# Performance work log

Measured on AMD Instinct MI355X. Metric: run time of the kernel, lower is better.

## Reference

```python
import jax, jax.numpy as jnp
import numpy as np

B, S, L = 512, 512, 128


def setup_inputs() -> dict:
    key = jax.random.key(0)
    k1, k2, k3, k4 = jax.random.split(key, 4)
    return {
        "input": jax.random.normal(k1, (B, S, L), dtype=jnp.float32),
        "label": jax.random.randint(k2, (B, S), 0, L),
        "length": jax.random.randint(k3, (B,), 1, S + 1),
        "trans": jax.random.uniform(k4, (L, L), dtype=jnp.float32),
    }


def reference(input, label, length, trans):
    b, s, l = input.shape
    length = jnp.clip(length, 1, s)
    # sequence mask [B, S]
    mask = (jnp.arange(s)[None, :] < length[:, None]).astype(input.dtype)
    x = input * mask[:, :, None]  # masked emissions, as in call()

    # --- gold path score (compute_path_score, via gathers instead of dense one-hot outer products) ---
    point_score = jnp.sum(
        jnp.take_along_axis(x, label[:, :, None], axis=2)[:, :, 0] * mask,
        axis=1, keepdims=True)
    pair_mask = mask[:, :-1] * mask[:, 1:]
    trans_score = jnp.sum(trans[label[:, :-1], label[:, 1:]] * pair_mask,
                          axis=1, keepdims=True)
    label_score = point_score + trans_score  # [B, 1]

    # --- forward algorithm (comput_z recurrence) as lax.scan ---
    def step(alpha, xt):
        # alpha: [B, L] prev forward vars; xt: [B, L] emissions at t
        alpha = jax.nn.logsumexp(alpha[:, :, None] + trans[None, :, :], axis=1) + xt
        return alpha, alpha

    alpha0 = x[:, 0, :]
    xs = jnp.swapaxes(x, 0, 1)[1:]  # [S-1, B, L]
    _, alphas = jax.lax.scan(step, alpha0, xs)
    alphas = jnp.concatenate([alpha0[None], alphas], axis=0)  # [S, B, L]

    # pick forward vars at the last valid position of each sequence
    final_scores = alphas[length - 1, jnp.arange(b)]  # [B, L]
    z = jax.nn.logsumexp(final_scores, axis=1, keepdims=True)  # [B, 1]
    return z - label_score
```

## Files before the change

kernel.cpp:

```cpp
#include <hip/hip_runtime.h>

#define BB 512
#define SS 512
#define LL 128

__global__ void __launch_bounds__(256) crf_label_score_kernel(
    const float* __restrict__ input, const int* __restrict__ label,
    const int* __restrict__ length, const float* __restrict__ trans,
    float* __restrict__ ls)
{
    const int b = blockIdx.x;
    const int tid = threadIdx.x;
    int len = length[b];
    len = len < 1 ? 1 : (len > SS ? SS : len);

    float acc = 0.f;
    for (int t = tid; t < len; t += 256) {
        const int lab = label[b * SS + t];
        acc += input[((size_t)b * SS + t) * LL + lab];
        if (t + 1 < len) {
            const int lab2 = label[b * SS + t + 1];
            acc += trans[lab * LL + lab2];
        }
    }
    #pragma unroll
    for (int off = 32; off > 0; off >>= 1) acc += __shfl_xor(acc, off, 64);
    __shared__ float wpart[4];
    if ((tid & 63) == 0) wpart[tid >> 6] = acc;
    __syncthreads();
    if (tid == 0) ls[b] = wpart[0] + wpart[1] + wpart[2] + wpart[3];
}

__global__ void __launch_bounds__(128) crf_forward_kernel(
    const float* __restrict__ input, const int* __restrict__ length,
    const float* __restrict__ trans, const float* __restrict__ ls,
    float* __restrict__ out)
{
    const int b = blockIdx.x;
    const int j = threadIdx.x;
    int len = length[b];
    len = len < 1 ? 1 : (len > SS ? SS : len);

    __shared__ float e_lds[LL];
    __shared__ float wred[2];
    __shared__ float wsum[2];

    float tcol[LL];
    #pragma unroll
    for (int i = 0; i < LL; ++i)
        tcol[i] = __expf(trans[i * LL + j]);

    const float* __restrict__ xb = input + (size_t)b * SS * LL;
    float alpha = xb[j];

    for (int t = 1; t < len; ++t) {
        const float xt = xb[t * LL + j];

        float m = alpha;
        #pragma unroll
        for (int off = 32; off > 0; off >>= 1) m = fmaxf(m, __shfl_xor(m, off, 64));
        if ((j & 63) == 0) wred[j >> 6] = m;
        __syncthreads();
        const float M = fmaxf(wred[0], wred[1]);

        e_lds[j] = __expf(alpha - M);
        __syncthreads();

        float acc0 = 0.f, acc1 = 0.f, acc2 = 0.f, acc3 = 0.f;
        const float4* __restrict__ e4 = reinterpret_cast<const float4*>(e_lds);
        #pragma unroll
        for (int i = 0; i < LL / 4; ++i) {
            const float4 ev = e4[i];
            acc0 = fmaf(ev.x, tcol[4 * i + 0], acc0);
            acc1 = fmaf(ev.y, tcol[4 * i + 1], acc1);
            acc2 = fmaf(ev.z, tcol[4 * i + 2], acc2);
            acc3 = fmaf(ev.w, tcol[4 * i + 3], acc3);
        }
        alpha = M + __logf((acc0 + acc1) + (acc2 + acc3)) + xt;
    }

    float m = alpha;
    #pragma unroll
    for (int off = 32; off > 0; off >>= 1) m = fmaxf(m, __shfl_xor(m, off, 64));
    if ((j & 63) == 0) wred[j >> 6] = m;
    __syncthreads();
    const float M = fmaxf(wred[0], wred[1]);

    float ex = __expf(alpha - M);
    #pragma unroll
    for (int off = 32; off > 0; off >>= 1) ex += __shfl_xor(ex, off, 64);
    if ((j & 63) == 0) wsum[j >> 6] = ex;
    __syncthreads();

    if (j == 0) out[b] = M + __logf(wsum[0] + wsum[1]) - ls[b];
}

extern "C" void kernel_launch(void* const* d_in, const int* in_sizes, int n_in,
                              void* d_out, int out_size, void* d_ws, size_t ws_size,
                              hipStream_t stream) {
    const float* input  = (const float*)d_in[0];
    const int*   label  = (const int*)d_in[1];
    const int*   length = (const int*)d_in[2];
    const float* trans  = (const float*)d_in[3];
    float* out = (float*)d_out;
    float* ls  = (float*)d_ws;

    crf_label_score_kernel<<<BB, 256, 0, stream>>>(input, label, length, trans, ls);
    crf_forward_kernel<<<BB, 128, 0, stream>>>(input, length, trans, ls, out);
}
```

Before: 683.4 us.

## Batch 16 sequences per block and run CRF forward recurrence on fp16 MFMA

Replaces the two kernels with one fused kernel in which each block handles 16 sequences. The per-step logsumexp matvec becomes an fp16 16x16x16 MFMA product with exp(trans) held in registers, instead of scalar FMAs per thread. It also uses a lagged max for stabilisation (previous step's max plus a safety margin) so each step needs one barrier, double-buffers LDS, and prefetches emissions three steps ahead. The cost is only 32 blocks on the GPU, fp16 rounding of exp values, possible overflow or underflow if alpha moves faster than the margin allows, and every block iterating to its longest sequence.

```diff
diff --git a/kernel.cpp b/kernel.cpp
--- a/kernel.cpp
+++ b/kernel.cpp
@@ -1,98 +1,210 @@
 #include <hip/hip_runtime.h>
 
-#define BB 512
 #define SS 512
-#define LL 128
-
-__global__ void __launch_bounds__(256) crf_label_score_kernel(
+#define LLc 128
+#define NB 16
+#define NG 32
+#define ROWB 272
+
+typedef __attribute__((ext_vector_type(4))) _Float16 half4;
+typedef __attribute__((ext_vector_type(4))) float float4v;
+
+static __device__ __forceinline__ unsigned short f2h(float f) {
+    _Float16 h = (_Float16)f;
+    unsigned short u;
+    __builtin_memcpy(&u, &h, 2);
+    return u;
+}
+
+__global__ void __launch_bounds__(256, 1) crf_mfma_kernel(
     const float* __restrict__ input, const int* __restrict__ label,
     const int* __restrict__ length, const float* __restrict__ trans,
-    float* __restrict__ ls)
-{
-    const int b = blockIdx.x;
-    const int tid = threadIdx.x;
-    int len = length[b];
-    len = len < 1 ? 1 : (len > SS ? SS : len);
-
-    float acc = 0.f;
-    for (int t = tid; t < len; t += 256) {
-        const int lab = label[b * SS + t];
-        acc += input[((size_t)b * SS + t) * LL + lab];
-        if (t + 1 < len) {
-            const int lab2 = label[b * SS + t + 1];
-            acc += trans[lab * LL + lab2];
-        }
-    }
-    #pragma unroll
-    for (int off = 32; off > 0; off >>= 1) acc += __shfl_xor(acc, off, 64);
-    __shared__ float wpart[4];
-    if ((tid & 63) == 0) wpart[tid >> 6] = acc;
-    __syncthreads();
-    if (tid == 0) ls[b] = wpart[0] + wpart[1] + wpart[2] + wpart[3];
-}
-
-__global__ void __launch_bounds__(128) crf_forward_kernel(
-    const float* __restrict__ input, const int* __restrict__ length,
-    const float* __restrict__ trans, const float* __restrict__ ls,
     float* __restrict__ out)
 {
-    const int b = blockIdx.x;
-    const int j = threadIdx.x;
-    int len = length[b];
-    len = len < 1 ? 1 : (len > SS ? SS : len);
-
-    __shared__ float e_lds[LL];
-    __shared__ float wred[2];
-    __shared__ float wsum[2];
-
-    float tcol[LL];
+    const int G    = blockIdx.x;
+    const int tid  = threadIdx.x;
+    const int w    = tid >> 6;
+    const int lane = tid & 63;
+    const int g16  = lane >> 4;
+    const int q    = lane & 15;
+    const int jb   = w * 32;
+
+    __shared__ __align__(16) unsigned char elds[2][NB * ROWB];
+    __shared__ __align__(16) float wmaxT[2][NB][4];
+    __shared__ float ls_lds[NB];
+
+    int lenq = length[G * NB + q];
+    lenq = lenq < 1 ? 1 : (lenq > SS ? SS : lenq);
+    int maxlen = lenq;
     #pragma unroll
-    for (int i = 0; i < LL; ++i)
-        tcol[i] = __expf(trans[i * LL + j]);
-
-    const float* __restrict__ xb = input + (size_t)b * SS * LL;
-    float alpha = xb[j];
-
-    for (int t = 1; t < len; ++t) {
-        const float xt = xb[t * LL + j];
-
-        float m = alpha;
-        #pragma unroll
-        for (int off = 32; off > 0; off >>= 1) m = fmaxf(m, __shfl_xor(m, off, 64));
-        if ((j & 63) == 0) wred[j >> 6] = m;
+    for (int off = 1; off < 16; off <<= 1)
+        maxlen = max(maxlen, __shfl_xor(maxlen, off, 64));
+
+    {
+        const int bl  = tid >> 4;
+        const int s16 = tid & 15;
+        int lenb = length[G * NB + bl];
+        lenb = lenb < 1 ? 1 : (lenb > SS ? SS : lenb);
+        const float* xb = input + (size_t)(G * NB + bl) * SS * LLc;
+        const int*   lb = label + (size_t)(G * NB + bl) * SS;
+        float acc = 0.f;
+        for (int t = s16; t < lenb; t += 16) {
+            const int la = lb[t];
+            acc += xb[(size_t)t * LLc + la];
+            if (t + 1 < lenb) acc += trans[la * LLc + lb[t + 1]];
+        }
+        #pragma unroll
+        for (int off = 1; off < 16; off <<= 1) acc += __shfl_xor(acc, off, 64);
+        if ((lane & 15) == 0) ls_lds[bl] = acc;
+    }
+
+    half4 afr[2][8];
+    #pragma unroll
+    for (int tt = 0; tt < 2; ++tt) {
+        const int j = jb + tt * 16 + q;
+        #pragma unroll
+        for (int kk = 0; kk < 8; ++kk) {
+            union { half4 v; unsigned short s[4]; } u;
+            #pragma unroll
+            for (int e = 0; e < 4; ++e) {
+                const int i = kk * 16 + g16 * 4 + e;
+                u.s[e] = f2h(__expf(trans[i * LLc + j]));
+            }
+            afr[tt][kk] = u.v;
+        }
+    }
+
+    const float* xq = input + (size_t)(G * NB + q) * SS * LLc;
+    const int j0 = jb + 4 * g16;
+    const int j1 = jb + 16 + 4 * g16;
+
+    float al[8];
+    {
+        float4v a0 = *(const float4v*)(xq + j0);
+        float4v a1 = *(const float4v*)(xq + j1);
+        #pragma unroll
+        for (int r = 0; r < 4; ++r) { al[r] = a0[r]; al[4 + r] = a1[r]; }
+    }
+
+    const float SAFE = 3.0f;
+
+    {
+        float m = al[0];
+        #pragma unroll
+        for (int k = 1; k < 8; ++k) m = fmaxf(m, al[k]);
+        m = fmaxf(m, __shfl_xor(m, 16, 64));
+        m = fmaxf(m, __shfl_xor(m, 32, 64));
+        if (g16 == 0) wmaxT[0][q][w] = m;
+    }
+    __syncthreads();
+    float M_add;
+    {
+        float4v mv = *(const float4v*)&wmaxT[0][q][0];
+        M_add = fmaxf(fmaxf(mv[0], mv[1]), fmaxf(mv[2], mv[3])) + SAFE;
+        #pragma unroll
+        for (int tt = 0; tt < 2; ++tt) {
+            unsigned u0 = (unsigned)f2h(__expf(al[tt*4+0] - M_add)) |
+                          ((unsigned)f2h(__expf(al[tt*4+1] - M_add)) << 16);
+            unsigned u1 = (unsigned)f2h(__expf(al[tt*4+2] - M_add)) |
+                          ((unsigned)f2h(__expf(al[tt*4+3] - M_add)) << 16);
+            const int jj = jb + tt * 16 + 4 * g16;
+            *(uint2*)(&elds[0][q * ROWB + jj * 2]) = make_uint2(u0, u1);
+        }
+    }
+    __syncthreads();
+
+    float4v xA[2], xB[2], xC[2];
+    {
+        const int t1 = 1 < maxlen ? 1 : maxlen - 1;
+        const int t2 = 2 < maxlen ? 2 : maxlen - 1;
+        const int t3 = 3 < maxlen ? 3 : maxlen - 1;
+        xA[0] = *(const float4v*)(xq + (size_t)t1 * LLc + j0);
+        xA[1] = *(const float4v*)(xq + (size_t)t1 * LLc + j1);
+        xB[0] = *(const float4v*)(xq + (size_t)t2 * LLc + j0);
+        xB[1] = *(const float4v*)(xq + (size_t)t2 * LLc + j1);
+        xC[0] = *(const float4v*)(xq + (size_t)t3 * LLc + j0);
+        xC[1] = *(const float4v*)(xq + (size_t)t3 * LLc + j1);
+    }
+
+    for (int t = 1; t < maxlen; ++t) {
+        const int cur = t & 1, prev = cur ^ 1;
+
+        int tf = t + 3; tf = tf < maxlen ? tf : maxlen - 1;
+        float4v xN0 = *(const float4v*)(xq + (size_t)tf * LLc + j0);
+        float4v xN1 = *(const float4v*)(xq + (size_t)tf * LLc + j1);
+
+        float4v mv = *(const float4v*)&wmaxT[prev][q][0];
+        const float Mst = fmaxf(fmaxf(mv[0], mv[1]), fmaxf(mv[2], mv[3]));
+
+        float4v acc0 = {0.f, 0.f, 0.f, 0.f};
+        float4v acc1 = {0.f, 0.f, 0.f, 0.f};
+        #pragma unroll
+        for (int kk = 0; kk < 8; ++kk) {
+            half4 bf = *(const half4*)(&elds[prev][q * ROWB + (kk * 16 + 4 * g16) * 2]);
+            acc0 = __builtin_amdgcn_mfma_f32_16x16x16f16(afr[0][kk], bf, acc0, 0, 0, 0);
+            acc1 = __builtin_amdgcn_mfma_f32_16x16x16f16(afr[1][kk], bf, acc1, 0, 0, 0);
+        }
+
+        const bool act = (t < lenq);
+        #pragma unroll
+        for (int r = 0; r < 4; ++r) {
+            const float n0 = M_add + __logf(acc0[r]) + xA[0][r];
+            const float n1 = M_add + __logf(acc1[r]) + xA[1][r];
+            al[r]     = act ? n0 : al[r];
+            al[4 + r] = act ? n1 : al[4 + r];
+        }
+        xA[0] = xB[0]; xA[1] = xB[1];
+        xB[0] = xC[0]; xB[1] = xC[1];
+        xC[0] = xN0;   xC[1] = xN1;
+
+        float mm = al[0];
+        #pragma unroll
+        for (int k = 1; k < 8; ++k) mm = fmaxf(mm, al[k]);
+        mm = fmaxf(mm, __shfl_xor(mm, 16, 64));
+        mm = fmaxf(mm, __shfl_xor(mm, 32, 64));
+        if (g16 == 0) wmaxT[cur][q][w] = mm;
+
+        const float Me = Mst + SAFE;
+        #pragma unroll
+        for (int tt = 0; tt < 2; ++tt) {
+            unsigned u0 = (unsigned)f2h(__expf(al[tt*4+0] - Me)) |
+                          ((unsigned)f2h(__expf(al[tt*4+1] - Me)) << 16);
+            unsigned u1 = (unsigned)f2h(__expf(al[tt*4+2] - Me)) |
+                          ((unsigned)f2h(__expf(al[tt*4+3] - Me)) << 16);
+            const int jj = jb + tt * 16 + 4 * g16;
+            *(uint2*)(&elds[cur][q * ROWB + jj * 2]) = make_uint2(u0, u1);
+        }
+        M_add = Me;
         __syncthreads();
-        const float M = fmaxf(wred[0], wred[1]);
-
-        e_lds[j] = __expf(alpha - M);
-        __syncthreads();
-
-        float acc0 = 0.f, acc1 = 0.f, acc2 = 0.f, acc3 = 0.f;
-        const float4* __restrict__ e4 = reinterpret_cast<const float4*>(e_lds);
-        #pragma unroll
-        for (int i = 0; i < LL / 4; ++i) {
-            const float4 ev = e4[i];
-            acc0 = fmaf(ev.x, tcol[4 * i + 0], acc0);
-            acc1 = fmaf(ev.y, tcol[4 * i + 1], acc1);
-            acc2 = fmaf(ev.z, tcol[4 * i + 2], acc2);
-            acc3 = fmaf(ev.w, tcol[4 * i + 3], acc3);
-        }
-        alpha = M + __logf((acc0 + acc1) + (acc2 + acc3)) + xt;
-    }
-
-    float m = alpha;
-    #pragma unroll
-    for (int off = 32; off > 0; off >>= 1) m = fmaxf(m, __shfl_xor(m, off, 64));
-    if ((j & 63) == 0) wred[j >> 6] = m;
-    __syncthreads();
-    const float M = fmaxf(wred[0], wred[1]);
-
-    float ex = __expf(alpha - M);
-    #pragma unroll
-    for (int off = 32; off > 0; off >>= 1) ex += __shfl_xor(ex, off, 64);
-    if ((j & 63) == 0) wsum[j >> 6] = ex;
-    __syncthreads();
-
-    if (j == 0) out[b] = M + __logf(wsum[0] + wsum[1]) - ls[b];
+    }
+
+    {
+        float mf = al[0];
+        #pragma unroll
+        for (int k = 1; k < 8; ++k) mf = fmaxf(mf, al[k]);
+        mf = fmaxf(mf, __shfl_xor(mf, 16, 64));
+        mf = fmaxf(mf, __shfl_xor(mf, 32, 64));
+        if (g16 == 0) wmaxT[0][q][w] = mf;
+    }
+    __syncthreads();
+    {
+        float4v mv = *(const float4v*)&wmaxT[0][q][0];
+        const float Mf = fmaxf(fmaxf(mv[0], mv[1]), fmaxf(mv[2], mv[3]));
+        float s = 0.f;
+        #pragma unroll
+        for (int k = 0; k < 8; ++k) s += __expf(al[k] - Mf);
+        s += __shfl_xor(s, 16, 64);
+        s += __shfl_xor(s, 32, 64);
+        if (g16 == 0) wmaxT[1][q][w] = s;
+    }
+    __syncthreads();
+    if (tid < NB) {
+        float4v mv = *(const float4v*)&wmaxT[0][tid][0];
+        const float Mf = fmaxf(fmaxf(mv[0], mv[1]), fmaxf(mv[2], mv[3]));
+        float4v sv = *(const float4v*)&wmaxT[1][tid][0];
+        const float z = Mf + __logf(sv[0] + sv[1] + sv[2] + sv[3]);
+        out[G * NB + tid] = z - ls_lds[tid];
+    }
 }
 
 extern "C" void kernel_launch(void* const* d_in, const int* in_sizes, int n_in,
@@ -103,8 +215,6 @@
     const int*   length = (const int*)d_in[2];
     const float* trans  = (const float*)d_in[3];
     float* out = (float*)d_out;
-    float* ls  = (float*)d_ws;
-
-    crf_label_score_kernel<<<BB, 256, 0, stream>>>(input, label, length, trans, ls);
-    crf_forward_kernel<<<BB, 128, 0, stream>>>(input, length, trans, ls, out);
+
+    crf_mfma_kernel<<<NG, 256, 0, stream>>>(input, label, length, trans, out);
 }
```

Measured after the change: 697.9 us. +2.1%, slower.
